# Kernel tuning notes

Measured on AMD Instinct MI355X. Metric: run time of the kernel, lower is better.

Reference implementation:

```python
import jax, jax.numpy as jnp
import numpy as np

N_NODES = 100000
N_EDGES = 800000
EDGE_NAMES = ["ei_connected_to", "ei_ordered_next", "ei_represents", "ei_represented_by",
              "ei_neighboring_vertical", "ei_neighboring_horizontal", "ei_contains",
              "ei_order", "ei_perpendicular"]
AGGRS_L2 = ["sum", "sum", "mean", "mean", "sum", "sum", "mean"]


def _glorot(key, shape):
    fan_in, fan_out = shape[-2], shape[-1]
    s = (2.0 / (fan_in + fan_out)) ** 0.5
    return jax.random.normal(key, shape, dtype=jnp.float32) * s


def setup_inputs() -> dict:
    key = jax.random.key(0)
    ks = iter(jax.random.split(key, 32))
    inp = {"x": jax.random.normal(next(ks), (N_NODES, 6), dtype=jnp.float32)}
    for name in EDGE_NAMES:
        inp[name] = jax.random.randint(next(ks), (2, N_EDGES), 0, N_NODES, dtype=jnp.int32)
    inp.update(
        W0n=_glorot(next(ks), (2, 6, 16)), W0r=_glorot(next(ks), (2, 6, 16)),
        b0=jnp.zeros((2, 16), jnp.float32),
        W1n=_glorot(next(ks), (2, 16, 32)), W1r=_glorot(next(ks), (2, 16, 32)),
        b1=jnp.zeros((2, 32), jnp.float32),
        P1=_glorot(next(ks), (16, 32)), pb1=jnp.zeros((32,), jnp.float32),
        W2n=_glorot(next(ks), (7, 32, 64)), W2r=_glorot(next(ks), (7, 32, 64)),
        b2=jnp.zeros((7, 64), jnp.float32),
        P2=_glorot(next(ks), (32, 64)), pb2=jnp.zeros((64,), jnp.float32),
    )
    return inp


def _hetero_conv(x, edges, aggrs, Wn, Wr, b):
    # Per-relation GraphConv: out_d = aggr(x[src]->dst) @ Wn_r + x @ Wr_r + b_r,
    # summed across relations (HeteroConv aggr='sum'). Loop is over a small fixed
    # set of relation types (structurally distinct), not data dims.
    n = x.shape[0]
    out = jnp.zeros((n, Wn.shape[-1]), x.dtype)
    for i, (ei, aggr) in enumerate(zip(edges, aggrs)):
        src, dst = ei[0], ei[1]
        msg = jax.ops.segment_sum(x[src], dst, num_segments=n)  # scatter-add gather
        if aggr == "mean":
            cnt = jax.ops.segment_sum(jnp.ones_like(dst, dtype=x.dtype), dst, num_segments=n)
            msg = msg / jnp.maximum(cnt, 1.0)[:, None]
        out = out + msg @ Wn[i] + x @ Wr[i] + b[i]
    return out


def reference(x, W0n, W0r, b0, W1n, W1r, b1, P1, pb1, W2n, W2r, b2, P2, pb2,
              ei_connected_to, ei_ordered_next, ei_represents, ei_represented_by,
              ei_neighboring_vertical, ei_neighboring_horizontal, ei_contains,
              ei_order, ei_perpendicular):
    e01 = [ei_connected_to, ei_ordered_next]
    e2 = [ei_represents, ei_represented_by, ei_neighboring_vertical,
          ei_neighboring_horizontal, ei_contains, ei_order, ei_perpendicular]
    # local head: 6 -> 16 (two sum relations)
    h = _hetero_conv(x, e01, ["sum", "sum"], W0n, W0r, b0)
    # residual block 1: 16 -> 32 (same two sum relations, linear residual projection)
    h = jax.nn.relu(_hetero_conv(h, e01, ["sum", "sum"], W1n, W1r, b1) + h @ P1 + pb1)
    # residual block 2: 32 -> 64 (seven relations, sum/mean aggregation)
    h = jax.nn.relu(_hetero_conv(h, e2, AGGRS_L2, W2n, W2r, b2) + h @ P2 + pb2)
    # final elementwise relu from SemanticModule.forward
    return jax.nn.relu(h)
```

## Files before the change

### kernel.cpp

```cpp
#include <hip/hip_runtime.h>

#define NN 100000
#define NE 800000
#define NRG 128
#define SPAN 784
#define CAP 8192
#define NBIN (9 * NRG)

typedef _Float16 f16;
typedef __attribute__((ext_vector_type(4))) _Float16 f16x4;
typedef __attribute__((ext_vector_type(8))) _Float16 f16x8;
typedef __attribute__((ext_vector_type(4))) float f32x4;
typedef __attribute__((ext_vector_type(2))) float f32x2;

struct EPtrs { const int* s[9]; const int* d[9]; };

__global__ __launch_bounds__(256) void prep_weights(
    const float* __restrict__ W0n, const float* __restrict__ W0r, const float* __restrict__ b0,
    const float* __restrict__ W1n, const float* __restrict__ W1r, const float* __restrict__ b1,
    const float* __restrict__ P1,  const float* __restrict__ pb1,
    const float* __restrict__ W2n, const float* __restrict__ W2r, const float* __restrict__ b2,
    const float* __restrict__ P2,  const float* __restrict__ pb2,
    float* __restrict__ wc0, float* __restrict__ bc0,
    float* __restrict__ wc1, float* __restrict__ bc1,
    f16*   __restrict__ b2frag, float* __restrict__ bc2,
    int*   __restrict__ cursor)
{
    int tid = threadIdx.x;
    for (int t = tid; t < NBIN; t += 256) cursor[t] = 0;

    for (int t = tid; t < 18 * 16; t += 256) {
        int row = t >> 4, col = t & 15;
        float v;
        if (row < 6)       v = W0n[row * 16 + col];
        else if (row < 12) v = W0n[96 + (row - 6) * 16 + col];
        else               v = W0r[(row - 12) * 16 + col] + W0r[96 + (row - 12) * 16 + col];
        wc0[t] = v;
    }
    for (int t = tid; t < 16; t += 256) bc0[t] = b0[t] + b0[16 + t];

    for (int t = tid; t < 48 * 32; t += 256) {
        int row = t >> 5, col = t & 31;
        float v;
        if (row < 16)      v = W1n[row * 32 + col];
        else if (row < 32) v = W1n[512 + (row - 16) * 32 + col];
        else { int rr = row - 32; v = W1r[rr * 32 + col] + W1r[512 + rr * 32 + col] + P1[rr * 32 + col]; }
        wc1[t] = v;
    }
    for (int t = tid; t < 32; t += 256) bc1[t] = b1[t] + b1[32 + t] + pb1[t];

    for (int t = tid; t < 256 * 64; t += 256) {
        int j = t & 7, lane = (t >> 3) & 63, ntk = t >> 9;
        int nt = ntk & 3, kt = ntk >> 2;
        int k = kt * 32 + (lane >> 4) * 8 + j;
        int n = nt * 16 + (lane & 15);
        float v;
        if (k < 224) v = W2n[k * 64 + n];
        else {
            int rr = k - 224;
            v = P2[rr * 64 + n];
            #pragma unroll
            for (int r = 0; r < 7; ++r) v += W2r[r * 2048 + rr * 64 + n];
        }
        b2frag[t] = (f16)v;
    }
    for (int t = tid; t < 64; t += 256) {
        float v = pb2[t];
        #pragma unroll
        for (int r = 0; r < 7; ++r) v += b2[r * 64 + t];
        bc2[t] = v;
    }
}

__global__ __launch_bounds__(256) void passA(EPtrs ep, int* __restrict__ cursor,
                                             unsigned* __restrict__ binbuf)
{
    int r = blockIdx.y;
    int e0 = blockIdx.x * 4096;
    int cnt = min(4096, NE - e0);
    int tid = threadIdx.x;
    __shared__ int h[NRG];
    __shared__ int bs[NRG + 1];
    __shared__ int cl[NRG];
    __shared__ int gb[NRG];
    __shared__ int auxtot;
    __shared__ unsigned pk[4096];

    if (tid < NRG) h[tid] = 0;
    __syncthreads();

    const int* dp = ep.d[r];
    const int* sp = ep.s[r];
    unsigned wv[16];
    int rgk[16];
    #pragma unroll
    for (int k = 0; k < 16; ++k) {
        int e = e0 + k * 256 + tid;
        rgk[k] = -1;
        if (e < NE) {
            int d = dp[e];
            int sv = sp[e];
            int g = d / SPAN;
            int l = d - g * SPAN;
            wv[k] = ((unsigned)l << 17) | (unsigned)sv;
            rgk[k] = g;
            atomicAdd(&h[g], 1);
        }
    }
    __syncthreads();

    int vcnt = 0, incl = 0;
    if (tid < NRG) {
        vcnt = h[tid];
        incl = vcnt;
        int lane = tid & 63;
        #pragma unroll
        for (int ofs = 1; ofs < 64; ofs <<= 1) {
            int u = __shfl_up(incl, ofs, 64);
            if (lane >= ofs) incl += u;
        }
        if (tid == 63) auxtot = incl;
    }
    __syncthreads();
    if (tid < NRG) {
        int excl = incl - vcnt + ((tid >= 64) ? auxtot : 0);
        bs[tid] = excl;
        cl[tid] = excl;
        gb[tid] = (vcnt > 0) ? atomicAdd(&cursor[r * NRG + tid], vcnt) : 0;
        if (tid == NRG - 1) bs[NRG] = excl + vcnt;
    }
    __syncthreads();

    #pragma unroll
    for (int k = 0; k < 16; ++k) {
        if (rgk[k] >= 0) {
            int p = atomicAdd(&cl[rgk[k]], 1);
            pk[p] = wv[k];
        }
    }
    __syncthreads();

    for (int i = tid; i < cnt; i += 256) {
        int loB = 0, hiB = NRG;
        while (hiB - loB > 1) {
            int mid = (loB + hiB) >> 1;
            if (bs[mid] <= i) loB = mid; else hiB = mid;
        }
        int b = loB;
        int pos = gb[b] + (i - bs[b]);
        if (pos < CAP)
            binbuf[((size_t)(r * NRG + b)) * CAP + pos] = pk[i];
    }
}

__global__ __launch_bounds__(256) void passB(const unsigned* __restrict__ binbuf,
                                             const int* __restrict__ cursor,
                                             int* __restrict__ deg, int* __restrict__ off,
                                             int* __restrict__ eidx)
{
    int bin = blockIdx.x;
    int r = bin >> 7, rg = bin & (NRG - 1);
    int lo = rg * SPAN;
    int n_here = min(SPAN, NN - lo);
    int tid = threadIdx.x;
    __shared__ int h[SPAN];
    __shared__ int wsum[4];
    __shared__ int stage[CAP];

    int sz = min(cursor[bin], CAP);
    const unsigned* bp = binbuf + (size_t)bin * CAP;

    for (int i = tid; i < SPAN; i += 256) h[i] = 0;
    __syncthreads();
    for (int e = tid; e < sz; e += 256) atomicAdd(&h[bp[e] >> 17], 1);
    __syncthreads();

    int i0 = tid * 4;
    int dstash[4];
    int s = 0;
    #pragma unroll
    for (int k = 0; k < 4; ++k) {
        int i = i0 + k;
        int v = (i < SPAN) ? h[i] : 0;
        dstash[k] = v;
        s += v;
    }
    int lane = tid & 63, wid = tid >> 6;
    int incl = s;
    #pragma unroll
    for (int ofs = 1; ofs < 64; ofs <<= 1) {
        int u = __shfl_up(incl, ofs, 64);
        if (lane >= ofs) incl += u;
    }
    if (lane == 63) wsum[wid] = incl;
    __syncthreads();
    if (tid == 0) {
        int a = wsum[0], b = wsum[1], c = wsum[2];
        wsum[0] = 0; wsum[1] = a; wsum[2] = a + b; wsum[3] = a + b + c;
    }
    __syncthreads();
    int run = incl - s + wsum[wid];
    int base = bin * CAP;
    #pragma unroll
    for (int k = 0; k < 4; ++k) {
        int i = i0 + k;
        if (i < SPAN) {
            int v = dstash[k];
            h[i] = run;
            if (i < n_here) {
                deg[r * NN + lo + i] = v;
                off[r * NN + lo + i] = base + run + v;
            }
            run += v;
        }
    }
    __syncthreads();

    for (int e = tid; e < sz; e += 256) {
        unsigned w = bp[e];
        int p = atomicAdd(&h[w >> 17], 1);
        stage[p] = (int)(w & 0x1FFFF);
    }
    __syncthreads();
    for (int i = tid; i < sz; i += 256) eidx[base + i] = stage[i];
}

__global__ __launch_bounds__(256, 2) void t0f(const float* __restrict__ x,
                                              const int* __restrict__ deg, const int* __restrict__ off,
                                              const int* __restrict__ eidx,
                                              const float* __restrict__ wc0, const float* __restrict__ bc0,
                                              f16* __restrict__ h0h)
{
    __shared__ float sw[288 + 16];
    for (int t = threadIdx.x; t < 304; t += 256) sw[t] = (t < 288) ? wc0[t] : bc0[t - 288];
    __syncthreads();
    int n = blockIdx.x * 256 + threadIdx.x;
    if (n >= NN) return;
    float acc[16];
    #pragma unroll
    for (int j = 0; j < 16; ++j) acc[j] = sw[288 + j];
    float xv[6];
    {
        const float2* xp = reinterpret_cast<const float2*>(x + (size_t)n * 6);
        float2 a = xp[0], b = xp[1], c = xp[2];
        xv[0] = a.x; xv[1] = a.y; xv[2] = b.x; xv[3] = b.y; xv[4] = c.x; xv[5] = c.y;
    }
    #pragma unroll
    for (int r = 0; r < 2; ++r) {
        float m[6] = {0, 0, 0, 0, 0, 0};
        int e1 = off[r * NN + n];
        int e0 = e1 - deg[r * NN + n];
        int e = e0;
        for (; e + 2 <= e1; e += 2) {
            int sA = eidx[e], sB = eidx[e + 1];
            const float2* pA = reinterpret_cast<const float2*>(x + (size_t)sA * 6);
            const float2* pB = reinterpret_cast<const float2*>(x + (size_t)sB * 6);
            float2 a0 = pA[0], a1 = pA[1], a2 = pA[2];
            float2 b0 = pB[0], b1 = pB[1], b2 = pB[2];
            m[0] += a0.x + b0.x; m[1] += a0.y + b0.y;
            m[2] += a1.x + b1.x; m[3] += a1.y + b1.y;
            m[4] += a2.x + b2.x; m[5] += a2.y + b2.y;
        }
        if (e < e1) {
            int sA = eidx[e];
            const float2* pA = reinterpret_cast<const float2*>(x + (size_t)sA * 6);
            float2 a0 = pA[0], a1 = pA[1], a2 = pA[2];
            m[0] += a0.x; m[1] += a0.y; m[2] += a1.x; m[3] += a1.y; m[4] += a2.x; m[5] += a2.y;
        }
        #pragma unroll
        for (int k = 0; k < 6; ++k) {
            float s = m[k];
            #pragma unroll
            for (int j = 0; j < 16; ++j) acc[j] = fmaf(s, sw[(r * 6 + k) * 16 + j], acc[j]);
        }
    }
    #pragma unroll
    for (int k = 0; k < 6; ++k) {
        float s = xv[k];
        #pragma unroll
        for (int j = 0; j < 16; ++j) acc[j] = fmaf(s, sw[(12 + k) * 16 + j], acc[j]);
    }
    f16x8 o0, o1;
    #pragma unroll
    for (int j = 0; j < 8; ++j) { o0[j] = (f16)acc[j]; o1[j] = (f16)acc[8 + j]; }
    f16x8* op = reinterpret_cast<f16x8*>(h0h + (size_t)n * 16);
    op[0] = o0; op[1] = o1;
}

__global__ __launch_bounds__(256) void g1(const int* __restrict__ deg, const int* __restrict__ off,
                                          const int* __restrict__ eidx, const f16* __restrict__ h0h,
                                          f16* __restrict__ msum)
{
    int t = blockIdx.x * 256 + threadIdx.x;
    int node = t >> 2, l = t & 3;
    if (node >= NN) return;
    int dd[2], oo[2];
    #pragma unroll
    for (int r = 0; r < 2; ++r) { dd[r] = deg[r * NN + node]; oo[r] = off[r * NN + node]; }
    #pragma unroll 1
    for (int r = 0; r < 2; ++r) {
        int e1 = oo[r];
        int e0 = e1 - dd[r];
        float a0 = 0.f, a1 = 0.f, a2 = 0.f, a3 = 0.f;
        int e = e0;
        for (; e + 4 <= e1; e += 4) {
            int sA = eidx[e], sB = eidx[e + 1], sC = eidx[e + 2], sD = eidx[e + 3];
            f16x4 vA = *reinterpret_cast<const f16x4*>(h0h + (size_t)sA * 16 + l * 4);
            f16x4 vB = *reinterpret_cast<const f16x4*>(h0h + (size_t)sB * 16 + l * 4);
            f16x4 vC = *reinterpret_cast<const f16x4*>(h0h + (size_t)sC * 16 + l * 4);
            f16x4 vD = *reinterpret_cast<const f16x4*>(h0h + (size_t)sD * 16 + l * 4);
            a0 += (float)vA[0] + (float)vB[0] + (float)vC[0] + (float)vD[0];
            a1 += (float)vA[1] + (float)vB[1] + (float)vC[1] + (float)vD[1];
            a2 += (float)vA[2] + (float)vB[2] + (float)vC[2] + (float)vD[2];
            a3 += (float)vA[3] + (float)vB[3] + (float)vC[3] + (float)vD[3];
        }
        for (; e < e1; ++e) {
            f16x4 v = *reinterpret_cast<const f16x4*>(h0h + (size_t)eidx[e] * 16 + l * 4);
            a0 += (float)v[0]; a1 += (float)v[1]; a2 += (float)v[2]; a3 += (float)v[3];
        }
        f16x4 o;
        o[0] = (f16)a0; o[1] = (f16)a1; o[2] = (f16)a2; o[3] = (f16)a3;
        *reinterpret_cast<f16x4*>(msum + (size_t)node * 32 + r * 16 + l * 4) = o;
    }
}

__global__ __launch_bounds__(256) void t1t(const f16* __restrict__ h0h, const f16* __restrict__ msum,
                                           const float* __restrict__ wc1, const float* __restrict__ bc1,
                                           f16* __restrict__ h1h, unsigned* __restrict__ h1q)
{
    __shared__ float sw[1536 + 32];
    for (int t = threadIdx.x; t < 1568; t += 256) sw[t] = (t < 1536) ? wc1[t] : bc1[t - 1536];
    __syncthreads();
    int n = blockIdx.x * 256 + threadIdx.x;
    if (n >= NN) return;
    float acc[32];
    #pragma unroll
    for (int j = 0; j < 32; ++j) acc[j] = sw[1536 + j];
    {
        const f16x8* mp = reinterpret_cast<const f16x8*>(msum + (size_t)n * 32);
        f16x8 m0 = mp[0], m1 = mp[1], m2 = mp[2], m3 = mp[3];
        #pragma unroll
        for (int k = 0; k < 8; ++k) {
            float s0 = (float)m0[k], s1 = (float)m1[k];
            float s2 = (float)m2[k], s3 = (float)m3[k];
            #pragma unroll
            for (int j = 0; j < 32; ++j)
                acc[j] += s0 * sw[k * 32 + j] + s1 * sw[(8 + k) * 32 + j]
                        + s2 * sw[(16 + k) * 32 + j] + s3 * sw[(24 + k) * 32 + j];
        }
    }
    {
        const f16x8* hp = reinterpret_cast<const f16x8*>(h0h + (size_t)n * 16);
        f16x8 a = hp[0], b = hp[1];
        #pragma unroll
        for (int k = 0; k < 8; ++k) {
            float s0 = (float)a[k], s1 = (float)b[k];
            #pragma unroll
            for (int j = 0; j < 32; ++j)
                acc[j] = fmaf(s0, sw[(32 + k) * 32 + j], fmaf(s1, sw[(40 + k) * 32 + j], acc[j]));
        }
    }
    #pragma unroll
    for (int j = 0; j < 32; ++j) acc[j] = fmaxf(acc[j], 0.f);

    f16x8* op = reinterpret_cast<f16x8*>(h1h + (size_t)n * 32);
    #pragma unroll
    for (int q = 0; q < 4; ++q) {
        f16x8 o;
        #pragma unroll
        for (int j = 0; j < 8; ++j) o[j] = (f16)acc[q * 8 + j];
        op[q] = o;
    }
    unsigned qw[8];
    #pragma unroll
    for (int q = 0; q < 8; ++q) {
        int w = __builtin_amdgcn_cvt_pk_fp8_f32(acc[q * 4 + 0], acc[q * 4 + 1], 0, false);
        w = __builtin_amdgcn_cvt_pk_fp8_f32(acc[q * 4 + 2], acc[q * 4 + 3], w, true);
        qw[q] = (unsigned)w;
    }
    uint4* qp = reinterpret_cast<uint4*>(h1q + (size_t)n * 8);
    qp[0] = make_uint4(qw[0], qw[1], qw[2], qw[3]);
    qp[1] = make_uint4(qw[4], qw[5], qw[6], qw[7]);
}

__global__ __launch_bounds__(256, 8) void g2t2(const int* __restrict__ deg, const int* __restrict__ off,
                                               const int* __restrict__ eidx, const unsigned* __restrict__ h1q,
                                               const f16* __restrict__ h1h, const f16* __restrict__ b2frag,
                                               const float* __restrict__ bc2, float* __restrict__ out)
{
    __shared__ f16 cat[16][264];

    int tid = threadIdx.x;
    int nloc = tid >> 4;
    int lane16 = tid & 15;
    int node = blockIdx.x * 16 + nloc;

    if (lane16 >= 14) {
        int part = lane16 - 14;
        const f16x8* hp = reinterpret_cast<const f16x8*>(h1h + (size_t)node * 32 + part * 16);
        f16x8 v0 = hp[0], v1 = hp[1];
        *reinterpret_cast<f16x8*>(&cat[nloc][224 + part * 16]) = v0;
        *reinterpret_cast<f16x8*>(&cat[nloc][224 + part * 16 + 8]) = v1;
    } else {
        int r = lane16 >> 1;
        int half = lane16 & 1;
        int d = deg[(r + 2) * NN + node];
        int e1 = off[(r + 2) * NN + node];
        int e0 = e1 - d;

        f32x2 acc[8];
        #pragma unroll
        for (int q = 0; q < 8; ++q) acc[q] = (f32x2){0.f, 0.f};

        const uint4* tbl = reinterpret_cast<const uint4*>(h1q);
        int e = e0;
        for (; e + 2 <= e1; e += 2) {
            int sA = eidx[e], sB = eidx[e + 1];
            uint4 qA = tbl[(size_t)sA * 2 + half];
            uint4 qB = tbl[(size_t)sB * 2 + half];
            acc[0] += __builtin_amdgcn_cvt_pk_f32_fp8(qA.x, false);
            acc[1] += __builtin_amdgcn_cvt_pk_f32_fp8(qA.x, true);
            acc[2] += __builtin_amdgcn_cvt_pk_f32_fp8(qA.y, false);
            acc[3] += __builtin_amdgcn_cvt_pk_f32_fp8(qA.y, true);
            acc[4] += __builtin_amdgcn_cvt_pk_f32_fp8(qA.z, false);
            acc[5] += __builtin_amdgcn_cvt_pk_f32_fp8(qA.z, true);
            acc[6] += __builtin_amdgcn_cvt_pk_f32_fp8(qA.w, false);
            acc[7] += __builtin_amdgcn_cvt_pk_f32_fp8(qA.w, true);
            acc[0] += __builtin_amdgcn_cvt_pk_f32_fp8(qB.x, false);
            acc[1] += __builtin_amdgcn_cvt_pk_f32_fp8(qB.x, true);
            acc[2] += __builtin_amdgcn_cvt_pk_f32_fp8(qB.y, false);
            acc[3] += __builtin_amdgcn_cvt_pk_f32_fp8(qB.y, true);
            acc[4] += __builtin_amdgcn_cvt_pk_f32_fp8(qB.z, false);
            acc[5] += __builtin_amdgcn_cvt_pk_f32_fp8(qB.z, true);
            acc[6] += __builtin_amdgcn_cvt_pk_f32_fp8(qB.w, false);
            acc[7] += __builtin_amdgcn_cvt_pk_f32_fp8(qB.w, true);
        }
        if (e < e1) {
            int sA = eidx[e];
            uint4 qA = tbl[(size_t)sA * 2 + half];
            acc[0] += __builtin_amdgcn_cvt_pk_f32_fp8(qA.x, false);
            acc[1] += __builtin_amdgcn_cvt_pk_f32_fp8(qA.x, true);
            acc[2] += __builtin_amdgcn_cvt_pk_f32_fp8(qA.y, false);
            acc[3] += __builtin_amdgcn_cvt_pk_f32_fp8(qA.y, true);
            acc[4] += __builtin_amdgcn_cvt_pk_f32_fp8(qA.z, false);
            acc[5] += __builtin_amdgcn_cvt_pk_f32_fp8(qA.z, true);
            acc[6] += __builtin_amdgcn_cvt_pk_f32_fp8(qA.w, false);
            acc[7] += __builtin_amdgcn_cvt_pk_f32_fp8(qA.w, true);
        }

        float sc = (r == 2 || r == 3 || r == 6) ? (1.0f / (float)max(d, 1)) : 1.0f;
        f16x8 o0, o1;
        #pragma unroll
        for (int q = 0; q < 4; ++q) {
            o0[q * 2 + 0] = (f16)(acc[q][0] * sc);
            o0[q * 2 + 1] = (f16)(acc[q][1] * sc);
            o1[q * 2 + 0] = (f16)(acc[4 + q][0] * sc);
            o1[q * 2 + 1] = (f16)(acc[4 + q][1] * sc);
        }
        *reinterpret_cast<f16x8*>(&cat[nloc][r * 32 + half * 16]) = o0;
        *reinterpret_cast<f16x8*>(&cat[nloc][r * 32 + half * 16 + 8]) = o1;
    }

    int lane = tid & 63, w = tid >> 6;
    int quad = lane >> 4, col0 = lane & 15;
    float bcv = bc2[w * 16 + col0];

    f16x8 bfr[8];
    #pragma unroll
    for (int kt = 0; kt < 8; ++kt)
        bfr[kt] = *reinterpret_cast<const f16x8*>(b2frag + ((size_t)(kt * 4 + w) * 64 + lane) * 8);

    __syncthreads();

    f32x4 acc = (f32x4){0.f, 0.f, 0.f, 0.f};
    #pragma unroll
    for (int kt = 0; kt < 8; ++kt) {
        f16x8 a = *reinterpret_cast<const f16x8*>(&cat[col0][kt * 32 + quad * 8]);
        acc = __builtin_amdgcn_mfma_f32_16x16x32_f16(a, bfr[kt], acc, 0, 0, 0);
    }

    int row0 = blockIdx.x * 16 + quad * 4;
    #pragma unroll
    for (int i = 0; i < 4; ++i)
        out[(size_t)(row0 + i) * 64 + w * 16 + col0] = fmaxf(acc[i] + bcv, 0.f);
}

extern "C" void kernel_launch(void* const* d_in, const int* in_sizes, int n_in,
                              void* d_out, int out_size, void* d_ws, size_t ws_size,
                              hipStream_t stream)
{
    const float* x = (const float*)d_in[0];
    EPtrs ep;
    for (int i = 0; i < 9; ++i) { const int* p = (const int*)d_in[1 + i]; ep.s[i] = p; ep.d[i] = p + NE; }
    const float* W0n = (const float*)d_in[10]; const float* W0r = (const float*)d_in[11];
    const float* b0  = (const float*)d_in[12];
    const float* W1n = (const float*)d_in[13]; const float* W1r = (const float*)d_in[14];
    const float* b1  = (const float*)d_in[15];
    const float* P1  = (const float*)d_in[16]; const float* pb1 = (const float*)d_in[17];
    const float* W2n = (const float*)d_in[18]; const float* W2r = (const float*)d_in[19];
    const float* b2  = (const float*)d_in[20];
    const float* P2  = (const float*)d_in[21]; const float* pb2 = (const float*)d_in[22];
    float* out = (float*)d_out;
    char* ws = (char*)d_ws;

    size_t off_b = 0;
    auto alloc = [&](size_t b) { size_t o = off_b; off_b += (b + 255) & ~(size_t)255; return o; };
    size_t o_wc0 = alloc(288 * 4);   size_t o_bc0 = alloc(16 * 4);
    size_t o_wc1 = alloc(1536 * 4);  size_t o_bc1 = alloc(32 * 4);
    size_t o_b2f = alloc(16384 * 2); size_t o_bc2 = alloc(64 * 4);
    size_t o_h0h = alloc((size_t)NN * 16 * 2);
    size_t o_h1q = alloc((size_t)NN * 32);
    size_t o_msum = alloc((size_t)NN * 32 * 2);
    size_t o_h1h = alloc((size_t)NN * 32 * 2);
    size_t o_bin = alloc((size_t)NBIN * CAP * 4);
    size_t o_deg = alloc((size_t)9 * NN * 4);
    size_t o_off = alloc((size_t)9 * NN * 4);
    size_t o_eid = alloc((size_t)NBIN * CAP * 4);
    size_t o_cur = alloc((size_t)NBIN * 4);
    (void)ws_size;

    float* wc0 = (float*)(ws + o_wc0); float* bc0 = (float*)(ws + o_bc0);
    float* wc1 = (float*)(ws + o_wc1); float* bc1 = (float*)(ws + o_bc1);
    f16*   b2f = (f16*)(ws + o_b2f);   float* bc2 = (float*)(ws + o_bc2);
    f16*   h0h = (f16*)(ws + o_h0h);
    unsigned* h1q = (unsigned*)(ws + o_h1q);
    f16*   msum = (f16*)(ws + o_msum);
    f16*   h1h = (f16*)(ws + o_h1h);
    unsigned* binbuf = (unsigned*)(ws + o_bin);
    int*   deg = (int*)(ws + o_deg);
    int*   offp = (int*)(ws + o_off);
    int*   eid = (int*)(ws + o_eid);
    int*   cur = (int*)(ws + o_cur);

    dim3 B(256);
    prep_weights<<<1, B, 0, stream>>>(W0n, W0r, b0, W1n, W1r, b1, P1, pb1,
                                      W2n, W2r, b2, P2, pb2,
                                      wc0, bc0, wc1, bc1, b2f, bc2, cur);
    passA<<<dim3((NE + 4095) / 4096, 9), B, 0, stream>>>(ep, cur, binbuf);
    passB<<<NBIN, B, 0, stream>>>(binbuf, cur, deg, offp, eid);

    t0f<<<(NN + 255) / 256, B, 0, stream>>>(x, deg, offp, eid, wc0, bc0, h0h);
    g1<<<(NN * 4 + 255) / 256, B, 0, stream>>>(deg, offp, eid, h0h, msum);
    t1t<<<(NN + 255) / 256, B, 0, stream>>>(h0h, msum, wc1, bc1, h1h, h1q);
    g2t2<<<NN / 16, B, 0, stream>>>(deg, offp, eid, h1q, h1h, b2f, bc2, out);
}
```

Measured before the change: 326.6 us.

## Fuse layer-1 gather with transform, widen t0f threads, drop LDS staging in binning

Layer-1 neighbor aggregation (g1) and its dense transform (t1t) become one kernel, g1t. It keeps per-node message sums in shared memory, so the fp16 msum round-trip through global memory and one launch go away. t0f now uses four threads per node: each relation's edge list is split in half and reduced with lane shuffles, which raises memory-level parallelism for the gather. passA and passB stop staging edges in LDS and scatter straight to final positions using the rank returned by the shared atomic. This saves LDS and syncs but makes the global writes less coalesced.

```diff
diff --git a/kernel.cpp b/kernel.cpp
--- a/kernel.cpp
+++ b/kernel.cpp
@@ -77,14 +77,9 @@
 {
     int r = blockIdx.y;
     int e0 = blockIdx.x * 4096;
-    int cnt = min(4096, NE - e0);
     int tid = threadIdx.x;
     __shared__ int h[NRG];
-    __shared__ int bs[NRG + 1];
-    __shared__ int cl[NRG];
     __shared__ int gb[NRG];
-    __shared__ int auxtot;
-    __shared__ unsigned pk[4096];
 
     if (tid < NRG) h[tid] = 0;
     __syncthreads();
@@ -93,6 +88,7 @@
     const int* sp = ep.s[r];
     unsigned wv[16];
     int rgk[16];
+    int lrk[16];
     #pragma unroll
     for (int k = 0; k < 16; ++k) {
         int e = e0 + k * 256 + tid;
@@ -104,52 +100,22 @@
             int l = d - g * SPAN;
             wv[k] = ((unsigned)l << 17) | (unsigned)sv;
             rgk[k] = g;
-            atomicAdd(&h[g], 1);
-        }
-    }
-    __syncthreads();
-
-    int vcnt = 0, incl = 0;
+            lrk[k] = atomicAdd(&h[g], 1);
+        }
+    }
+    __syncthreads();
     if (tid < NRG) {
-        vcnt = h[tid];
-        incl = vcnt;
-        int lane = tid & 63;
-        #pragma unroll
-        for (int ofs = 1; ofs < 64; ofs <<= 1) {
-            int u = __shfl_up(incl, ofs, 64);
-            if (lane >= ofs) incl += u;
-        }
-        if (tid == 63) auxtot = incl;
-    }
-    __syncthreads();
-    if (tid < NRG) {
-        int excl = incl - vcnt + ((tid >= 64) ? auxtot : 0);
-        bs[tid] = excl;
-        cl[tid] = excl;
-        gb[tid] = (vcnt > 0) ? atomicAdd(&cursor[r * NRG + tid], vcnt) : 0;
-        if (tid == NRG - 1) bs[NRG] = excl + vcnt;
-    }
-    __syncthreads();
-
+        int v = h[tid];
+        gb[tid] = (v > 0) ? atomicAdd(&cursor[r * NRG + tid], v) : 0;
+    }
+    __syncthreads();
     #pragma unroll
     for (int k = 0; k < 16; ++k) {
         if (rgk[k] >= 0) {
-            int p = atomicAdd(&cl[rgk[k]], 1);
-            pk[p] = wv[k];
-        }
-    }
-    __syncthreads();
-
-    for (int i = tid; i < cnt; i += 256) {
-        int loB = 0, hiB = NRG;
-        while (hiB - loB > 1) {
-            int mid = (loB + hiB) >> 1;
-            if (bs[mid] <= i) loB = mid; else hiB = mid;
-        }
-        int b = loB;
-        int pos = gb[b] + (i - bs[b]);
-        if (pos < CAP)
-            binbuf[((size_t)(r * NRG + b)) * CAP + pos] = pk[i];
+            int p = gb[rgk[k]] + lrk[k];
+            if (p < CAP)
+                binbuf[((size_t)(r * NRG + rgk[k])) * CAP + p] = wv[k];
+        }
     }
 }
 
@@ -165,14 +131,24 @@
     int tid = threadIdx.x;
     __shared__ int h[SPAN];
     __shared__ int wsum[4];
-    __shared__ int stage[CAP];
 
     int sz = min(cursor[bin], CAP);
     const unsigned* bp = binbuf + (size_t)bin * CAP;
 
     for (int i = tid; i < SPAN; i += 256) h[i] = 0;
     __syncthreads();
-    for (int e = tid; e < sz; e += 256) atomicAdd(&h[bp[e] >> 17], 1);
+
+    unsigned wv[32];
+    int rk[32];
+    #pragma unroll
+    for (int k = 0; k < 32; ++k) {
+        int e = tid + k * 256;
+        if (e < sz) {
+            unsigned w = bp[e];
+            wv[k] = w;
+            rk[k] = atomicAdd(&h[w >> 17], 1);
+        }
+    }
     __syncthreads();
 
     int i0 = tid * 4;
@@ -216,43 +192,38 @@
     }
     __syncthreads();
 
-    for (int e = tid; e < sz; e += 256) {
-        unsigned w = bp[e];
-        int p = atomicAdd(&h[w >> 17], 1);
-        stage[p] = (int)(w & 0x1FFFF);
-    }
-    __syncthreads();
-    for (int i = tid; i < sz; i += 256) eidx[base + i] = stage[i];
-}
-
-__global__ __launch_bounds__(256, 2) void t0f(const float* __restrict__ x,
-                                              const int* __restrict__ deg, const int* __restrict__ off,
-                                              const int* __restrict__ eidx,
-                                              const float* __restrict__ wc0, const float* __restrict__ bc0,
-                                              f16* __restrict__ h0h)
+    #pragma unroll
+    for (int k = 0; k < 32; ++k) {
+        int e = tid + k * 256;
+        if (e < sz) {
+            unsigned w = wv[k];
+            eidx[base + h[w >> 17] + rk[k]] = (int)(w & 0x1FFFF);
+        }
+    }
+}
+
+__global__ __launch_bounds__(256) void t0f(const float* __restrict__ x,
+                                           const int* __restrict__ deg, const int* __restrict__ off,
+                                           const int* __restrict__ eidx,
+                                           const float* __restrict__ wc0, const float* __restrict__ bc0,
+                                           f16* __restrict__ h0h)
 {
     __shared__ float sw[288 + 16];
     for (int t = threadIdx.x; t < 304; t += 256) sw[t] = (t < 288) ? wc0[t] : bc0[t - 288];
     __syncthreads();
-    int n = blockIdx.x * 256 + threadIdx.x;
-    if (n >= NN) return;
-    float acc[16];
-    #pragma unroll
-    for (int j = 0; j < 16; ++j) acc[j] = sw[288 + j];
-    float xv[6];
+    int t = blockIdx.x * 256 + threadIdx.x;
+    int node = t >> 2;
+    if (node >= NN) return;
+    int l = t & 3;
+    int r = l >> 1, p = l & 1;
+
+    float m[6] = {0, 0, 0, 0, 0, 0};
     {
-        const float2* xp = reinterpret_cast<const float2*>(x + (size_t)n * 6);
-        float2 a = xp[0], b = xp[1], c = xp[2];
-        xv[0] = a.x; xv[1] = a.y; xv[2] = b.x; xv[3] = b.y; xv[4] = c.x; xv[5] = c.y;
-    }
-    #pragma unroll
-    for (int r = 0; r < 2; ++r) {
-        float m[6] = {0, 0, 0, 0, 0, 0};
-        int e1 = off[r * NN + n];
-        int e0 = e1 - deg[r * NN + n];
-        int e = e0;
-        for (; e + 2 <= e1; e += 2) {
-            int sA = eidx[e], sB = eidx[e + 1];
+        int e1 = off[r * NN + node];
+        int e0 = e1 - deg[r * NN + node];
+        int e = e0 + p;
+        for (; e + 2 < e1; e += 4) {
+            int sA = eidx[e], sB = eidx[e + 2];
             const float2* pA = reinterpret_cast<const float2*>(x + (size_t)sA * 6);
             const float2* pB = reinterpret_cast<const float2*>(x + (size_t)sB * 6);
             float2 a0 = pA[0], a1 = pA[1], a2 = pA[2];
@@ -267,120 +238,117 @@
             float2 a0 = pA[0], a1 = pA[1], a2 = pA[2];
             m[0] += a0.x; m[1] += a0.y; m[2] += a1.x; m[3] += a1.y; m[4] += a2.x; m[5] += a2.y;
         }
+    }
+    float mo[6];
+    #pragma unroll
+    for (int k = 0; k < 6; ++k) {
+        m[k] += __shfl_xor(m[k], 1, 64);
+        mo[k] = __shfl_xor(m[k], 2, 64);
+    }
+    int baseOwn = r * 96, baseOth = (1 - r) * 96;
+    float xv[6];
+    {
+        const float2* xp = reinterpret_cast<const float2*>(x + (size_t)node * 6);
+        float2 a = xp[0], b = xp[1], c = xp[2];
+        xv[0] = a.x; xv[1] = a.y; xv[2] = b.x; xv[3] = b.y; xv[4] = c.x; xv[5] = c.y;
+    }
+    int dc = l * 4;
+    float acc[4];
+    #pragma unroll
+    for (int j = 0; j < 4; ++j) acc[j] = sw[288 + dc + j];
+    #pragma unroll
+    for (int k = 0; k < 6; ++k) {
         #pragma unroll
-        for (int k = 0; k < 6; ++k) {
-            float s = m[k];
-            #pragma unroll
-            for (int j = 0; j < 16; ++j) acc[j] = fmaf(s, sw[(r * 6 + k) * 16 + j], acc[j]);
-        }
-    }
-    #pragma unroll
-    for (int k = 0; k < 6; ++k) {
-        float s = xv[k];
-        #pragma unroll
-        for (int j = 0; j < 16; ++j) acc[j] = fmaf(s, sw[(12 + k) * 16 + j], acc[j]);
-    }
-    f16x8 o0, o1;
-    #pragma unroll
-    for (int j = 0; j < 8; ++j) { o0[j] = (f16)acc[j]; o1[j] = (f16)acc[8 + j]; }
-    f16x8* op = reinterpret_cast<f16x8*>(h0h + (size_t)n * 16);
-    op[0] = o0; op[1] = o1;
-}
-
-__global__ __launch_bounds__(256) void g1(const int* __restrict__ deg, const int* __restrict__ off,
-                                          const int* __restrict__ eidx, const f16* __restrict__ h0h,
-                                          f16* __restrict__ msum)
-{
-    int t = blockIdx.x * 256 + threadIdx.x;
-    int node = t >> 2, l = t & 3;
-    if (node >= NN) return;
-    int dd[2], oo[2];
-    #pragma unroll
-    for (int r = 0; r < 2; ++r) { dd[r] = deg[r * NN + node]; oo[r] = off[r * NN + node]; }
-    #pragma unroll 1
-    for (int r = 0; r < 2; ++r) {
-        int e1 = oo[r];
-        int e0 = e1 - dd[r];
-        float a0 = 0.f, a1 = 0.f, a2 = 0.f, a3 = 0.f;
-        int e = e0;
-        for (; e + 4 <= e1; e += 4) {
-            int sA = eidx[e], sB = eidx[e + 1], sC = eidx[e + 2], sD = eidx[e + 3];
-            f16x4 vA = *reinterpret_cast<const f16x4*>(h0h + (size_t)sA * 16 + l * 4);
-            f16x4 vB = *reinterpret_cast<const f16x4*>(h0h + (size_t)sB * 16 + l * 4);
-            f16x4 vC = *reinterpret_cast<const f16x4*>(h0h + (size_t)sC * 16 + l * 4);
-            f16x4 vD = *reinterpret_cast<const f16x4*>(h0h + (size_t)sD * 16 + l * 4);
-            a0 += (float)vA[0] + (float)vB[0] + (float)vC[0] + (float)vD[0];
-            a1 += (float)vA[1] + (float)vB[1] + (float)vC[1] + (float)vD[1];
-            a2 += (float)vA[2] + (float)vB[2] + (float)vC[2] + (float)vD[2];
-            a3 += (float)vA[3] + (float)vB[3] + (float)vC[3] + (float)vD[3];
-        }
-        for (; e < e1; ++e) {
-            f16x4 v = *reinterpret_cast<const f16x4*>(h0h + (size_t)eidx[e] * 16 + l * 4);
-            a0 += (float)v[0]; a1 += (float)v[1]; a2 += (float)v[2]; a3 += (float)v[3];
-        }
-        f16x4 o;
-        o[0] = (f16)a0; o[1] = (f16)a1; o[2] = (f16)a2; o[3] = (f16)a3;
-        *reinterpret_cast<f16x4*>(msum + (size_t)node * 32 + r * 16 + l * 4) = o;
-    }
-}
-
-__global__ __launch_bounds__(256) void t1t(const f16* __restrict__ h0h, const f16* __restrict__ msum,
+        for (int j = 0; j < 4; ++j) {
+            acc[j] = fmaf(m[k],  sw[baseOwn + k * 16 + dc + j], acc[j]);
+            acc[j] = fmaf(mo[k], sw[baseOth + k * 16 + dc + j], acc[j]);
+            acc[j] = fmaf(xv[k], sw[192 + k * 16 + dc + j], acc[j]);
+        }
+    }
+    f16x4 o;
+    #pragma unroll
+    for (int j = 0; j < 4; ++j) o[j] = (f16)acc[j];
+    *reinterpret_cast<f16x4*>(h0h + (size_t)node * 16 + dc) = o;
+}
+
+__global__ __launch_bounds__(256) void g1t(const int* __restrict__ deg, const int* __restrict__ off,
+                                           const int* __restrict__ eidx, const f16* __restrict__ h0h,
                                            const float* __restrict__ wc1, const float* __restrict__ bc1,
                                            f16* __restrict__ h1h, unsigned* __restrict__ h1q)
 {
     __shared__ float sw[1536 + 32];
+    __shared__ float ms[64][33];
     for (int t = threadIdx.x; t < 1568; t += 256) sw[t] = (t < 1536) ? wc1[t] : bc1[t - 1536];
-    __syncthreads();
-    int n = blockIdx.x * 256 + threadIdx.x;
-    if (n >= NN) return;
-    float acc[32];
-    #pragma unroll
-    for (int j = 0; j < 32; ++j) acc[j] = sw[1536 + j];
+
+    int tid = threadIdx.x;
+    int nloc = tid >> 2, l = tid & 3;
+    int node = blockIdx.x * 64 + nloc;
+
+    if (node < NN) {
+        #pragma unroll 1
+        for (int r = 0; r < 2; ++r) {
+            int e1 = off[r * NN + node];
+            int e0 = e1 - deg[r * NN + node];
+            float a0 = 0.f, a1 = 0.f, a2 = 0.f, a3 = 0.f;
+            int e = e0;
+            for (; e + 4 <= e1; e += 4) {
+                int sA = eidx[e], sB = eidx[e + 1], sC = eidx[e + 2], sD = eidx[e + 3];
+                f16x4 vA = *reinterpret_cast<const f16x4*>(h0h + (size_t)sA * 16 + l * 4);
+                f16x4 vB = *reinterpret_cast<const f16x4*>(h0h + (size_t)sB * 16 + l * 4);
+                f16x4 vC = *reinterpret_cast<const f16x4*>(h0h + (size_t)sC * 16 + l * 4);
+                f16x4 vD = *reinterpret_cast<const f16x4*>(h0h + (size_t)sD * 16 + l * 4);
+                a0 += (float)vA[0] + (float)vB[0] + (float)vC[0] + (float)vD[0];
+                a1 += (float)vA[1] + (float)vB[1] + (float)vC[1] + (float)vD[1];
+                a2 += (float)vA[2] + (float)vB[2] + (float)vC[2] + (float)vD[2];
+                a3 += (float)vA[3] + (float)vB[3] + (float)vC[3] + (float)vD[3];
+            }
+            for (; e < e1; ++e) {
+                f16x4 v = *reinterpret_cast<const f16x4*>(h0h + (size_t)eidx[e] * 16 + l * 4);
+                a0 += (float)v[0]; a1 += (float)v[1]; a2 += (float)v[2]; a3 += (float)v[3];
+            }
+            ms[nloc][r * 16 + l * 4 + 0] = a0;
+            ms[nloc][r * 16 + l * 4 + 1] = a1;
+            ms[nloc][r * 16 + l * 4 + 2] = a2;
+            ms[nloc][r * 16 + l * 4 + 3] = a3;
+        }
+    }
+    __syncthreads();
+    if (node >= NN) return;
+
+    int c0 = l * 8;
+    float acc[8];
+    #pragma unroll
+    for (int j = 0; j < 8; ++j) acc[j] = sw[1536 + c0 + j];
+    #pragma unroll
+    for (int k = 0; k < 32; ++k) {
+        float s = ms[nloc][k];
+        #pragma unroll
+        for (int j = 0; j < 8; ++j) acc[j] = fmaf(s, sw[k * 32 + c0 + j], acc[j]);
+    }
     {
-        const f16x8* mp = reinterpret_cast<const f16x8*>(msum + (size_t)n * 32);
-        f16x8 m0 = mp[0], m1 = mp[1], m2 = mp[2], m3 = mp[3];
-        #pragma unroll
-        for (int k = 0; k < 8; ++k) {
-            float s0 = (float)m0[k], s1 = (float)m1[k];
-            float s2 = (float)m2[k], s3 = (float)m3[k];
-            #pragma unroll
-            for (int j = 0; j < 32; ++j)
-                acc[j] += s0 * sw[k * 32 + j] + s1 * sw[(8 + k) * 32 + j]
-                        + s2 * sw[(16 + k) * 32 + j] + s3 * sw[(24 + k) * 32 + j];
-        }
-    }
-    {
-        const f16x8* hp = reinterpret_cast<const f16x8*>(h0h + (size_t)n * 16);
+        const f16x8* hp = reinterpret_cast<const f16x8*>(h0h + (size_t)node * 16);
         f16x8 a = hp[0], b = hp[1];
         #pragma unroll
         for (int k = 0; k < 8; ++k) {
             float s0 = (float)a[k], s1 = (float)b[k];
             #pragma unroll
-            for (int j = 0; j < 32; ++j)
-                acc[j] = fmaf(s0, sw[(32 + k) * 32 + j], fmaf(s1, sw[(40 + k) * 32 + j], acc[j]));
-        }
-    }
-    #pragma unroll
-    for (int j = 0; j < 32; ++j) acc[j] = fmaxf(acc[j], 0.f);
-
-    f16x8* op = reinterpret_cast<f16x8*>(h1h + (size_t)n * 32);
-    #pragma unroll
-    for (int q = 0; q < 4; ++q) {
-        f16x8 o;
-        #pragma unroll
-        for (int j = 0; j < 8; ++j) o[j] = (f16)acc[q * 8 + j];
-        op[q] = o;
-    }
-    unsigned qw[8];
-    #pragma unroll
-    for (int q = 0; q < 8; ++q) {
-        int w = __builtin_amdgcn_cvt_pk_fp8_f32(acc[q * 4 + 0], acc[q * 4 + 1], 0, false);
-        w = __builtin_amdgcn_cvt_pk_fp8_f32(acc[q * 4 + 2], acc[q * 4 + 3], w, true);
-        qw[q] = (unsigned)w;
-    }
-    uint4* qp = reinterpret_cast<uint4*>(h1q + (size_t)n * 8);
-    qp[0] = make_uint4(qw[0], qw[1], qw[2], qw[3]);
-    qp[1] = make_uint4(qw[4], qw[5], qw[6], qw[7]);
+            for (int j = 0; j < 8; ++j)
+                acc[j] = fmaf(s0, sw[(32 + k) * 32 + c0 + j], fmaf(s1, sw[(40 + k) * 32 + c0 + j], acc[j]));
+        }
+    }
+    #pragma unroll
+    for (int j = 0; j < 8; ++j) acc[j] = fmaxf(acc[j], 0.f);
+
+    f16x8 o;
+    #pragma unroll
+    for (int j = 0; j < 8; ++j) o[j] = (f16)acc[j];
+    *reinterpret_cast<f16x8*>(h1h + (size_t)node * 32 + c0) = o;
+
+    int w0 = __builtin_amdgcn_cvt_pk_fp8_f32(acc[0], acc[1], 0, false);
+    w0 = __builtin_amdgcn_cvt_pk_fp8_f32(acc[2], acc[3], w0, true);
+    int w1 = __builtin_amdgcn_cvt_pk_fp8_f32(acc[4], acc[5], 0, false);
+    w1 = __builtin_amdgcn_cvt_pk_fp8_f32(acc[6], acc[7], w1, true);
+    *reinterpret_cast<uint2*>(h1q + (size_t)node * 8 + l * 2) = make_uint2((unsigned)w0, (unsigned)w1);
 }
 
 __global__ __launch_bounds__(256, 8) void g2t2(const int* __restrict__ deg, const int* __restrict__ off,
@@ -510,7 +478,6 @@
     size_t o_b2f = alloc(16384 * 2); size_t o_bc2 = alloc(64 * 4);
     size_t o_h0h = alloc((size_t)NN * 16 * 2);
     size_t o_h1q = alloc((size_t)NN * 32);
-    size_t o_msum = alloc((size_t)NN * 32 * 2);
     size_t o_h1h = alloc((size_t)NN * 32 * 2);
     size_t o_bin = alloc((size_t)NBIN * CAP * 4);
     size_t o_deg = alloc((size_t)9 * NN * 4);
@@ -524,7 +491,6 @@
     f16*   b2f = (f16*)(ws + o_b2f);   float* bc2 = (float*)(ws + o_bc2);
     f16*   h0h = (f16*)(ws + o_h0h);
     unsigned* h1q = (unsigned*)(ws + o_h1q);
-    f16*   msum = (f16*)(ws + o_msum);
     f16*   h1h = (f16*)(ws + o_h1h);
     unsigned* binbuf = (unsigned*)(ws + o_bin);
     int*   deg = (int*)(ws + o_deg);
@@ -539,8 +505,7 @@
     passA<<<dim3((NE + 4095) / 4096, 9), B, 0, stream>>>(ep, cur, binbuf);
     passB<<<NBIN, B, 0, stream>>>(binbuf, cur, deg, offp, eid);
 
-    t0f<<<(NN + 255) / 256, B, 0, stream>>>(x, deg, offp, eid, wc0, bc0, h0h);
-    g1<<<(NN * 4 + 255) / 256, B, 0, stream>>>(deg, offp, eid, h0h, msum);
-    t1t<<<(NN + 255) / 256, B, 0, stream>>>(h0h, msum, wc1, bc1, h1h, h1q);
+    t0f<<<(NN * 4 + 255) / 256, B, 0, stream>>>(x, deg, offp, eid, wc0, bc0, h0h);
+    g1t<<<(NN + 63) / 64, B, 0, stream>>>(deg, offp, eid, h0h, wc1, bc1, h1h, h1q);
     g2t2<<<NN / 16, B, 0, stream>>>(deg, offp, eid, h1q, h1h, b2f, bc2, out);
 }
```

After: 334.9 us. 1.03x slower.
